# Kernel optimization log

Measured on AMD Instinct MI355X. Metric: run time of the kernel, lower is better.

The kernel has to match this reference:

```python
import jax, jax.numpy as jnp
import numpy as np

K = 1024
D = 256
BETA = 0.25


def setup_inputs() -> dict:
    key = jax.random.key(0)
    kx, kc = jax.random.split(key)
    x = jax.random.normal(kx, (64, 32, 32, D), dtype=jnp.float32)
    limit = 1.0 / K
    codebook = jax.random.uniform(kc, (K, D), dtype=jnp.float32, minval=-limit, maxval=limit)
    return {"x": x, "codebook": codebook}


def reference(x, codebook):
    flat = x.reshape(-1, D)                                   # [N, D]
    x2 = jnp.sum(jnp.square(flat), axis=1, keepdims=True)     # [N, 1]
    e2 = jnp.sum(jnp.square(codebook), axis=1)                # [K]
    sim = flat @ codebook.T                                   # [N, K]
    dist = x2 + e2 - 2.0 * sim                                # [N, K]
    idx = jnp.argmin(dist, axis=1)                            # [N]
    q = codebook[idx].reshape(x.shape)                        # [..., D]

    q_st = jax.lax.stop_gradient(q)
    x_st = jax.lax.stop_gradient(x)
    commit = jnp.mean(jnp.square(q_st - x))
    codebk = jnp.mean(jnp.square(q - x_st))
    loss = BETA * commit + codebk

    # code-usage statistics via histogram (equivalent to mean of one-hot)
    counts = jnp.zeros((K,), dtype=x.dtype).at[idx].add(1.0)
    probs = counts / flat.shape[0]
    eps = jnp.asarray(1e-10, dtype=x.dtype)
    H = -jnp.sum(probs * jnp.log2(probs + eps))               # bits/index
    perplexity = jnp.exp(H * jnp.log(jnp.asarray(2.0, dtype=x.dtype)))
    usage = jnp.sum((probs > 0).astype(x.dtype)) / float(K)

    y = x + jax.lax.stop_gradient(q - x)                      # straight-through
    return y, idx, loss, perplexity, usage, H
```

## Files before the change

### kernel.cpp

```cpp
#include <hip/hip_runtime.h>
#include <math.h>

#define D       256
#define KCODES  1024
#define NROWS   65536
#define BETA    0.25f
#define MARGIN  1e-3f
#define MAXSURV 7

typedef __attribute__((ext_vector_type(8))) short bf16x8;
typedef __attribute__((ext_vector_type(4))) float f32x4;

__device__ __forceinline__ unsigned int bf16_rne(float f) {
    unsigned int u = __float_as_uint(f);
    return (u + 0x7FFFu + ((u >> 16) & 1u)) >> 16;
}
__device__ __forceinline__ f32x4 mfma16(bf16x8 a, bf16x8 b, f32x4 c) {
    return __builtin_amdgcn_mfma_f32_16x16x32_bf16(a, b, c, 0, 0, 0);
}

__global__ __launch_bounds__(256) void split_cb_kernel(const float* __restrict__ cb,
                                                       ushort* __restrict__ cs,
                                                       float* __restrict__ e2f) {
    int code = blockIdx.x * 4 + (threadIdx.x >> 6);
    int lane = threadIdx.x & 63;
    float4 v = ((const float4*)(cb + (size_t)code * D))[lane];
    double s = (double)v.x * v.x + (double)v.y * v.y +
               (double)v.z * v.z + (double)v.w * v.w;
    ushort* ph = cs + (size_t)code * 256 + lane * 4;
    ph[0] = (ushort)bf16_rne(v.x); ph[1] = (ushort)bf16_rne(v.y);
    ph[2] = (ushort)bf16_rne(v.z); ph[3] = (ushort)bf16_rne(v.w);
    #pragma unroll
    for (int off = 32; off > 0; off >>= 1) s += __shfl_down(s, off, 64);
    if (lane == 0) e2f[code] = (float)s;
}

__global__ __launch_bounds__(512, 4) void screen_kernel(
    const float* __restrict__ x, const ushort* __restrict__ cs,
    const float* __restrict__ e2f, float* __restrict__ x2f,
    ushort* __restrict__ rowlist)
{
    __shared__ __attribute__((aligned(16))) ushort Bt[2][32 * 264];
    unsigned* mrg = (unsigned*)&Bt[0][0];
    #define MRG(r, j) mrg[(r) * 33 + (j)]

    const int tid  = threadIdx.x;
    const int wave = tid >> 6, lane = tid & 63;
    const int quad = lane >> 4, m = lane & 15;
    const int rowBase = blockIdx.x * 128;
    const int wrb = rowBase + wave * 16;

    const int sc = tid & 31, sp = tid >> 5;
    bf16x8 stg[2];
    {
        const ushort* src = cs + (size_t)sc * 256 + sp * 16;
        stg[0] = *(const bf16x8*)&src[0];
        stg[1] = *(const bf16x8*)&src[8];
    }

    bf16x8 af[8];
    {
        const float* xr = x + (size_t)(wrb + m) * D;
        double s = 0.0;
        #pragma unroll
        for (int c = 0; c < 8; ++c) {
            float4 f0 = *(const float4*)&xr[c * 32 + quad * 8];
            float4 f1 = *(const float4*)&xr[c * 32 + quad * 8 + 4];
            s += (double)f0.x * f0.x + (double)f0.y * f0.y +
                 (double)f0.z * f0.z + (double)f0.w * f0.w;
            s += (double)f1.x * f1.x + (double)f1.y * f1.y +
                 (double)f1.z * f1.z + (double)f1.w * f1.w;
            float ff[8] = {f0.x, f0.y, f0.z, f0.w, f1.x, f1.y, f1.z, f1.w};
            #pragma unroll
            for (int j = 0; j < 8; ++j) af[c][j] = (short)bf16_rne(ff[j]);
        }
        s += __shfl_xor(s, 16, 64);
        s += __shfl_xor(s, 32, 64);
        if (quad == 0) x2f[wrb + m] = (float)s;
    }

    unsigned u1[4], u2[4];
    #pragma unroll
    for (int r = 0; r < 4; ++r) { u1[r] = 0xFFFFFFFFu; u2[r] = 0xFFFFFFFFu; }

    for (int kt = 0; kt < KCODES / 32; ++kt) {
        {
            ushort* dst = &Bt[kt & 1][sc * 264 + sp * 16];
            *(bf16x8*)&dst[0] = stg[0];
            *(bf16x8*)&dst[8] = stg[1];
        }
        __syncthreads();
        if (kt < KCODES / 32 - 1) {
            const ushort* src = cs + (size_t)((kt + 1) * 32 + sc) * 256 + sp * 16;
            stg[0] = *(const bf16x8*)&src[0];
            stg[1] = *(const bf16x8*)&src[8];
        }

        float e2pa = e2f[kt * 32 + m] + 0.5f;
        float e2pb = e2f[kt * 32 + 16 + m] + 0.5f;

        const ushort* Bcur = &Bt[kt & 1][0];
        #pragma unroll
        for (int nt = 0; nt < 2; ++nt) {
            f32x4 acc = {0.f, 0.f, 0.f, 0.f};
            const ushort* bp = Bcur + (nt * 16 + m) * 264 + quad * 8;
            __builtin_amdgcn_s_setprio(1);
            #pragma unroll
            for (int c = 0; c < 8; ++c) {
                bf16x8 bh = *(const bf16x8*)&bp[c * 32];
                acc = mfma16(af[c], bh, acc);
            }
            __builtin_amdgcn_s_setprio(0);
            unsigned kcode = kt * 32 + nt * 16 + m;
            float e2p = nt ? e2pb : e2pa;
            #pragma unroll
            for (int r = 0; r < 4; ++r) {
                float d = fmaf(-2.f, acc[r], e2p);
                unsigned u = (__float_as_uint(d) & 0xFFFFFC00u) | kcode;
                bool lt1 = u < u1[r];
                bool lt2 = u < u2[r];
                u2[r] = lt2 ? (lt1 ? u1[r] : u) : u2[r];
                u1[r] = lt1 ? u : u1[r];
            }
        }
    }

    #pragma unroll
    for (int r = 0; r < 4; ++r) {
        int rowloc = wave * 16 + quad * 4 + r;
        MRG(rowloc, m * 2 + 0) = u1[r];
        MRG(rowloc, m * 2 + 1) = u2[r];
    }
    __syncthreads();
    if (tid < 128) {
        unsigned umin = 0xFFFFFFFFu;
        #pragma unroll
        for (int j = 0; j < 32; ++j) umin = min(umin, MRG(tid, j));
        float dfloor = __uint_as_float(umin & 0xFFFFFC00u);
        unsigned limu = (__float_as_uint(dfloor + MARGIN) & 0xFFFFFC00u) | 1023u;
        ushort out[8] = {0, 0, 0, 0, 0, 0, 0, 0};
        int cnt = 0;
        for (int j = 0; j < 32; ++j) {
            unsigned u = MRG(tid, j);
            if (u <= limu && cnt < MAXSURV) { out[1 + cnt] = (ushort)(u & 1023u); ++cnt; }
        }
        out[0] = (ushort)cnt;
        *(bf16x8*)&rowlist[(size_t)(rowBase + tid) * 8] = *(bf16x8*)out;
    }
    #undef MRG
}

__global__ __launch_bounds__(256) void rescore_kernel(
    const float* __restrict__ x, const float* __restrict__ cb,
    const float* __restrict__ x2f, const float* __restrict__ e2f,
    const ushort* __restrict__ rowlist, float* __restrict__ out_idxf,
    unsigned int* __restrict__ counts, float* __restrict__ y,
    float* __restrict__ msepart)
{
    int row  = blockIdx.x * 4 + (threadIdx.x >> 6);
    int lane = threadIdx.x & 63;
    const ushort* lst = rowlist + (size_t)row * 8;
    int cnt = lst[0];
    float4 xv = ((const float4*)(x + (size_t)row * D))[lane];

    int bk;
    if (cnt == 1) {
        bk = lst[1];
    } else {
        float x2 = x2f[row];
        float bestd = 1e30f;
        int   bestk = 0;
        for (int s = 0; s < cnt; ++s) {
            int k = lst[1 + s];
            float4 cv = ((const float4*)(cb + (size_t)k * D))[lane];
            double p = (double)xv.x * cv.x + (double)xv.y * cv.y +
                       (double)xv.z * cv.z + (double)xv.w * cv.w;
            #pragma unroll
            for (int off = 32; off > 0; off >>= 1) p += __shfl_down(p, off, 64);
            float simf = (float)p;
            float tt   = x2 + e2f[k];
            float dq   = tt - 2.0f * simf;
            if (dq < bestd || (dq == bestd && k < bestk)) { bestd = dq; bestk = k; }
        }
        bk = __shfl(bestk, 0, 64);
    }
    if (lane == 0) {
        out_idxf[row] = (float)bk;
        atomicAdd(&counts[bk], 1u);
    }
    float4 q = ((const float4*)(cb + (size_t)bk * D))[lane];
    float4 dv;
    dv.x = q.x - xv.x; dv.y = q.y - xv.y; dv.z = q.z - xv.z; dv.w = q.w - xv.w;
    float4 yv;
    yv.x = xv.x + dv.x; yv.y = xv.y + dv.y; yv.z = xv.z + dv.z; yv.w = xv.w + dv.w;
    ((float4*)(y + (size_t)row * D))[lane] = yv;
    float s = dv.x * dv.x + dv.y * dv.y + dv.z * dv.z + dv.w * dv.w;
    #pragma unroll
    for (int off = 32; off > 0; off >>= 1) s += __shfl_down(s, off, 64);
    if (lane == 0) msepart[row] = s;
}

__global__ __launch_bounds__(1024) void stats_kernel(
    const unsigned int* __restrict__ counts, const float* __restrict__ msepart,
    float* __restrict__ outs)
{
    int t = threadIdx.x;
    float ms = 0.f;
    #pragma unroll
    for (int j = 0; j < 64; ++j) ms += msepart[t + 1024 * j];

    float p = (float)counts[t] * (1.0f / 65536.0f);
    float h = -p * log2f(p + 1e-10f);
    float u = (p > 0.f) ? 1.f : 0.f;
    #pragma unroll
    for (int off = 32; off > 0; off >>= 1) {
        h  += __shfl_down(h,  off, 64);
        u  += __shfl_down(u,  off, 64);
        ms += __shfl_down(ms, off, 64);
    }
    __shared__ float hs[16], us[16], mss[16];
    int lane = t & 63, w = t >> 6;
    if (lane == 0) { hs[w] = h; us[w] = u; mss[w] = ms; }
    __syncthreads();
    if (t == 0) {
        float H = 0.f, U = 0.f, M = 0.f;
        #pragma unroll
        for (int i = 0; i < 16; ++i) { H += hs[i]; U += us[i]; M += mss[i]; }
        float m = M * (1.0f / 16777216.0f);
        float loss = BETA * m + m;
        float perp = expf(H * 0.69314718055994530942f);
        outs[0] = loss;
        outs[1] = perp;
        outs[2] = U * (1.0f / 1024.0f);
        outs[3] = H;
    }
}

extern "C" void kernel_launch(void* const* d_in, const int* in_sizes, int n_in,
                              void* d_out, int out_size, void* d_ws, size_t ws_size,
                              hipStream_t stream) {
    const float* x  = (const float*)d_in[0];
    const float* cb = (const float*)d_in[1];
    float* out      = (float*)d_out;

    float* y        = out;
    float* out_idxf = out + 16777216;
    float* outs     = out + 16777216 + 65536;

    float*        x2f     = (float*)d_ws;
    float*        e2f     = (float*)((char*)d_ws + 262144);
    unsigned int* counts  = (unsigned int*)((char*)d_ws + 266240);
    ushort*       rowlist = (ushort*)((char*)d_ws + 270400);
    ushort*       cs      = (ushort*)((char*)d_ws + 1318976);
    float*        msepart = (float*)((char*)d_ws + 1843264);

    hipMemsetAsync((char*)d_ws + 266240, 0, 4096, stream);
    split_cb_kernel<<<KCODES / 4, 256, 0, stream>>>(cb, cs, e2f);
    screen_kernel<<<NROWS / 128, 512, 0, stream>>>(x, cs, e2f, x2f, rowlist);
    rescore_kernel<<<NROWS / 4, 256, 0, stream>>>(x, cb, x2f, e2f, rowlist,
                                                  out_idxf, counts, y, msepart);
    stats_kernel<<<1, 1024, 0, stream>>>(counts, msepart, outs);
}
```

Measured before the change: 198.4 us.

## Fuse rescore and output pass into screen kernel epilogue

The separate rescore kernel is merged into the screening kernel. Each block keeps its candidate lists and row norms in shared memory, and each wave then rescores 16 rows, writes y, idx, counts and MSE partials. This removes a kernel launch and the global round trip of rowlist and x2f, and it rereads x while it is likely still in cache. In exchange, the epilogue's memory-bound work runs at the screen kernel's occupancy and per-block parallelism rather than as a widely parallel standalone kernel.

Measured after the change: 191.9 us. -3.3%, faster.

```diff
diff --git a/kernel.cpp b/kernel.cpp
--- a/kernel.cpp
+++ b/kernel.cpp
@@ -37,10 +37,12 @@
 
 __global__ __launch_bounds__(512, 4) void screen_kernel(
     const float* __restrict__ x, const ushort* __restrict__ cs,
-    const float* __restrict__ e2f, float* __restrict__ x2f,
-    ushort* __restrict__ rowlist)
+    const float* __restrict__ e2f, const float* __restrict__ cb,
+    float* __restrict__ out_idxf, unsigned int* __restrict__ counts,
+    float* __restrict__ y, float* __restrict__ msepart)
 {
     __shared__ __attribute__((aligned(16))) ushort Bt[2][32 * 264];
+    __shared__ float x2s[128];
     unsigned* mrg = (unsigned*)&Bt[0][0];
     #define MRG(r, j) mrg[(r) * 33 + (j)]
 
@@ -76,7 +78,7 @@
         }
         s += __shfl_xor(s, 16, 64);
         s += __shfl_xor(s, 32, 64);
-        if (quad == 0) x2f[wrb + m] = (float)s;
+        if (quad == 0) x2s[wave * 16 + m] = (float)s;
     }
 
     unsigned u1[4], u2[4];
@@ -145,59 +147,55 @@
             if (u <= limu && cnt < MAXSURV) { out[1 + cnt] = (ushort)(u & 1023u); ++cnt; }
         }
         out[0] = (ushort)cnt;
-        *(bf16x8*)&rowlist[(size_t)(rowBase + tid) * 8] = *(bf16x8*)out;
+        *(bf16x8*)&mrg[tid * 33] = *(bf16x8*)out;
+    }
+    __syncthreads();
+
+    #pragma unroll 2
+    for (int i = 0; i < 16; ++i) {
+        int rl  = wave * 16 + i;
+        int row = rowBase + rl;
+        const ushort* lst = (const ushort*)&mrg[rl * 33];
+        int cnt = lst[0];
+        float4 xv = ((const float4*)(x + (size_t)row * D))[lane];
+
+        int bk;
+        if (cnt == 1) {
+            bk = lst[1];
+        } else {
+            float x2 = x2s[rl];
+            float bestd = 1e30f;
+            int   bestk = 0;
+            for (int s = 0; s < cnt; ++s) {
+                int k = lst[1 + s];
+                float4 cv = ((const float4*)(cb + (size_t)k * D))[lane];
+                double p = (double)xv.x * cv.x + (double)xv.y * cv.y +
+                           (double)xv.z * cv.z + (double)xv.w * cv.w;
+                #pragma unroll
+                for (int off = 32; off > 0; off >>= 1) p += __shfl_down(p, off, 64);
+                float simf = (float)p;
+                float tt   = x2 + e2f[k];
+                float dq   = tt - 2.0f * simf;
+                if (dq < bestd || (dq == bestd && k < bestk)) { bestd = dq; bestk = k; }
+            }
+            bk = __shfl(bestk, 0, 64);
+        }
+        if (lane == 0) {
+            out_idxf[row] = (float)bk;
+            atomicAdd(&counts[bk], 1u);
+        }
+        float4 q = ((const float4*)(cb + (size_t)bk * D))[lane];
+        float4 dv;
+        dv.x = q.x - xv.x; dv.y = q.y - xv.y; dv.z = q.z - xv.z; dv.w = q.w - xv.w;
+        float4 yv;
+        yv.x = xv.x + dv.x; yv.y = xv.y + dv.y; yv.z = xv.z + dv.z; yv.w = xv.w + dv.w;
+        ((float4*)(y + (size_t)row * D))[lane] = yv;
+        float s = dv.x * dv.x + dv.y * dv.y + dv.z * dv.z + dv.w * dv.w;
+        #pragma unroll
+        for (int off = 32; off > 0; off >>= 1) s += __shfl_down(s, off, 64);
+        if (lane == 0) msepart[row] = s;
     }
     #undef MRG
-}
-
-__global__ __launch_bounds__(256) void rescore_kernel(
-    const float* __restrict__ x, const float* __restrict__ cb,
-    const float* __restrict__ x2f, const float* __restrict__ e2f,
-    const ushort* __restrict__ rowlist, float* __restrict__ out_idxf,
-    unsigned int* __restrict__ counts, float* __restrict__ y,
-    float* __restrict__ msepart)
-{
-    int row  = blockIdx.x * 4 + (threadIdx.x >> 6);
-    int lane = threadIdx.x & 63;
-    const ushort* lst = rowlist + (size_t)row * 8;
-    int cnt = lst[0];
-    float4 xv = ((const float4*)(x + (size_t)row * D))[lane];
-
-    int bk;
-    if (cnt == 1) {
-        bk = lst[1];
-    } else {
-        float x2 = x2f[row];
-        float bestd = 1e30f;
-        int   bestk = 0;
-        for (int s = 0; s < cnt; ++s) {
-            int k = lst[1 + s];
-            float4 cv = ((const float4*)(cb + (size_t)k * D))[lane];
-            double p = (double)xv.x * cv.x + (double)xv.y * cv.y +
-                       (double)xv.z * cv.z + (double)xv.w * cv.w;
-            #pragma unroll
-            for (int off = 32; off > 0; off >>= 1) p += __shfl_down(p, off, 64);
-            float simf = (float)p;
-            float tt   = x2 + e2f[k];
-            float dq   = tt - 2.0f * simf;
-            if (dq < bestd || (dq == bestd && k < bestk)) { bestd = dq; bestk = k; }
-        }
-        bk = __shfl(bestk, 0, 64);
-    }
-    if (lane == 0) {
-        out_idxf[row] = (float)bk;
-        atomicAdd(&counts[bk], 1u);
-    }
-    float4 q = ((const float4*)(cb + (size_t)bk * D))[lane];
-    float4 dv;
-    dv.x = q.x - xv.x; dv.y = q.y - xv.y; dv.z = q.z - xv.z; dv.w = q.w - xv.w;
-    float4 yv;
-    yv.x = xv.x + dv.x; yv.y = xv.y + dv.y; yv.z = xv.z + dv.z; yv.w = xv.w + dv.w;
-    ((float4*)(y + (size_t)row * D))[lane] = yv;
-    float s = dv.x * dv.x + dv.y * dv.y + dv.z * dv.z + dv.w * dv.w;
-    #pragma unroll
-    for (int off = 32; off > 0; off >>= 1) s += __shfl_down(s, off, 64);
-    if (lane == 0) msepart[row] = s;
 }
 
 __global__ __launch_bounds__(1024) void stats_kernel(
@@ -247,17 +245,14 @@
     float* out_idxf = out + 16777216;
     float* outs     = out + 16777216 + 65536;
 
-    float*        x2f     = (float*)d_ws;
     float*        e2f     = (float*)((char*)d_ws + 262144);
     unsigned int* counts  = (unsigned int*)((char*)d_ws + 266240);
-    ushort*       rowlist = (ushort*)((char*)d_ws + 270400);
     ushort*       cs      = (ushort*)((char*)d_ws + 1318976);
     float*        msepart = (float*)((char*)d_ws + 1843264);
 
     hipMemsetAsync((char*)d_ws + 266240, 0, 4096, stream);
     split_cb_kernel<<<KCODES / 4, 256, 0, stream>>>(cb, cs, e2f);
-    screen_kernel<<<NROWS / 128, 512, 0, stream>>>(x, cs, e2f, x2f, rowlist);
-    rescore_kernel<<<NROWS / 4, 256, 0, stream>>>(x, cb, x2f, e2f, rowlist,
-                                                  out_idxf, counts, y, msepart);
+    screen_kernel<<<NROWS / 128, 512, 0, stream>>>(x, cs, e2f, cb,
+                                                   out_idxf, counts, y, msepart);
     stats_kernel<<<1, 1024, 0, stream>>>(counts, msepart, outs);
 }
```
